# Optimization experiments

Measured on AMD Instinct MI355X. Metric: run time of the kernel, lower is better.

The kernel has to match this reference:

```python
import jax, jax.numpy as jnp
import numpy as np

N = 100000
E = 1600000
DIM = 16
H = 128


def setup_inputs() -> dict:
    key = jax.random.key(0)
    ks = jax.random.split(key, 16)
    s = 0.05
    inp = {
        "x": jax.random.normal(ks[0], (N, DIM), dtype=jnp.float32),
        "edge_index": jax.random.randint(ks[1], (2, E), 0, N, dtype=jnp.int32),
        # mlp_pre: dim -> h -> h -> h (ReLU after each, incl. last)
        "W1": jax.random.normal(ks[2], (DIM, H), dtype=jnp.float32) * s,
        "b1": jnp.zeros((H,), jnp.float32),
        "W2": jax.random.normal(ks[3], (H, H), dtype=jnp.float32) * s,
        "b2": jnp.zeros((H,), jnp.float32),
        "W3": jax.random.normal(ks[4], (H, H), dtype=jnp.float32) * s,
        "b3": jnp.zeros((H,), jnp.float32),
        # lin: h -> h (message transform)
        "Wl": jax.random.normal(ks[5], (H, H), dtype=jnp.float32) * s,
        "bl": jnp.zeros((H,), jnp.float32),
        # mlp_post: 2h -> h -> h -> dim (ReLU after first two only)
        "P1": jax.random.normal(ks[6], (2 * H, H), dtype=jnp.float32) * s,
        "pb1": jnp.zeros((H,), jnp.float32),
        "P2": jax.random.normal(ks[7], (H, H), dtype=jnp.float32) * s,
        "pb2": jnp.zeros((H,), jnp.float32),
        "P3": jax.random.normal(ks[8], (H, DIM), dtype=jnp.float32) * s,
        "pb3": jnp.zeros((DIM,), jnp.float32),
    }
    return inp


def _mlp_pre(x, W1, b1, W2, b2, W3, b3):
    h = jax.nn.relu(x @ W1 + b1)
    h = jax.nn.relu(h @ W2 + b2)
    return jax.nn.relu(h @ W3 + b3)


def reference(x, edge_index, W1, b1, W2, b2, W3, b3, Wl, bl, P1, pb1, P2, pb2, P3, pb3):
    # mlp_pre and the message transform are pointwise per node, so compute once
    # per node, then gather per edge (same math as PyG's per-edge x_j path).
    pre = _mlp_pre(x, W1, b1, W2, b2, W3, b3)            # [N, H]
    msg_node = jax.nn.relu(pre @ Wl + bl)                # [N, H]
    src, dst = edge_index[0], edge_index[1]
    agg = jax.ops.segment_sum(msg_node[src], dst, num_segments=N)  # [N, H]
    h = jnp.concatenate([pre, agg], axis=1)              # [N, 2H]
    h = jax.nn.relu(h @ P1 + pb1)
    h = jax.nn.relu(h @ P2 + pb2)
    out = h @ P3 + pb3                                   # [N, DIM] (no last act in mlp_post)
    return jax.nn.relu(out)                              # outer activation in GNNCASimple
```

## Files before the change

### kernel.cpp

```cpp
#include <hip/hip_runtime.h>

#define N_ 100000
#define E_ 1600000
#define HD 128
#define NB 391
#define GB 256
#define CHK 6250
#define NBGB (NB * GB)

typedef unsigned short u16;
typedef unsigned int u32;
typedef __bf16 bf16x8 __attribute__((ext_vector_type(8)));
typedef float f32x4 __attribute__((ext_vector_type(4)));

#define OFF_W2 0
#define OFF_W3 16384
#define OFF_WL 32768
#define OFF_P2 49152
#define OFF_P1 65536
#define PK_TOT 98304

__device__ __forceinline__ u16 f2bf(float f) {
    u32 u = __float_as_uint(f);
    return (u16)((u + 0x7FFFu + ((u >> 16) & 1u)) >> 16);
}
__device__ __forceinline__ float bf2f(u16 h) {
    return __uint_as_float(((u32)h) << 16);
}
__device__ __forceinline__ f32x4 mfma16(uint4 a, uint4 b, f32x4 c) {
    return __builtin_amdgcn_mfma_f32_16x16x32_bf16(
        __builtin_bit_cast(bf16x8, a), __builtin_bit_cast(bf16x8, b), c, 0, 0, 0);
}

__device__ __forceinline__ uint4 ldsA(const u16* A, int row, int kt, int l) {
    int idx = row * 128 + (((kt * 32 + ((l >> 4) << 3))) ^ ((row & 7) << 3));
    return *(const uint4*)&A[idx];
}

__device__ __forceinline__ void writeActH(u16* Ah, f32x4 acc, int mt, int nt, int l) {
    const int col = nt * 16 + (l & 15);
#pragma unroll
    for (int r = 0; r < 4; ++r) {
        const int row = mt * 16 + ((l >> 4) << 2) + r;
        Ah[row * 128 + (col ^ ((row & 7) << 3))] = f2bf(fmaxf(acc[r], 0.f));
    }
}

template<int MT, int KT>
__device__ __forceinline__ void mfmaLayerW(const u16* Ah,
                                           const u16* __restrict__ wph,
                                           const u16* __restrict__ wpl,
                                           const float* __restrict__ bias,
                                           int nt, int l, f32x4 acc[MT])
{
    const float bv = bias[nt * 16 + (l & 15)];
#pragma unroll
    for (int mt = 0; mt < MT; ++mt) {
        acc[mt][0] = bv; acc[mt][1] = bv; acc[mt][2] = bv; acc[mt][3] = bv;
    }
#pragma unroll
    for (int kt = 0; kt < KT; ++kt) {
        uint4 bh = *(const uint4*)&wph[((nt * KT + kt) * 64 + l) * 8];
        uint4 bl = *(const uint4*)&wpl[((nt * KT + kt) * 64 + l) * 8];
#pragma unroll
        for (int mt = 0; mt < MT; ++mt) {
            uint4 ah = ldsA(Ah, mt * 16 + (l & 15), kt, l);
            acc[mt] = mfma16(ah, bl, acc[mt]);
            acc[mt] = mfma16(ah, bh, acc[mt]);
        }
    }
}

__global__ __launch_bounds__(256) void k_pack(
    const float* __restrict__ W2, const float* __restrict__ W3,
    const float* __restrict__ Wl, const float* __restrict__ P2,
    const float* __restrict__ P1, u16* __restrict__ wpk)
{
    int e = blockIdx.x * 256 + threadIdx.x;
    if (e >= PK_TOT) return;
    const float* src; int local, KT;
    if (e < OFF_P1) {
        int m = e >> 14;
        src = (m == 0) ? W2 : (m == 1) ? W3 : (m == 2) ? Wl : P2;
        local = e & 16383; KT = 4;
    } else {
        src = P1; local = e - OFF_P1; KT = 8;
    }
    int j = local & 7, lane = (local >> 3) & 63, t = local >> 9;
    int kt = t % KT, nt = t / KT;
    int k = kt * 32 + ((lane >> 4) << 3) + j;
    int n = nt * 16 + (lane & 15);
    float v = src[k * HD + n];
    u16 h = f2bf(v);
    wpk[e] = h;
    wpk[PK_TOT + e] = f2bf(v - bf2f(h));
}

template<int NPH>
__device__ __forceinline__ void layer1(const float xs[][16],
                                       const float* __restrict__ W1,
                                       const float* __restrict__ b1,
                                       u16* Uh, int f, int g)
{
    float w[16];
#pragma unroll
    for (int j = 0; j < 16; ++j) w[j] = W1[j * HD + f];
    const float bb = b1[f];
#pragma unroll
    for (int nn = 0; nn < NPH; ++nn) {
        const int row = g * NPH + nn;
        const float4* h4 = (const float4*)xs[row];
        float4 h0 = h4[0], h1 = h4[1], h2 = h4[2], h3 = h4[3];
        float a = bb
            + h0.x * w[0] + h0.y * w[1] + h0.z * w[2] + h0.w * w[3]
            + h1.x * w[4] + h1.y * w[5] + h1.z * w[6] + h1.w * w[7]
            + h2.x * w[8] + h2.y * w[9] + h2.z * w[10] + h2.w * w[11]
            + h3.x * w[12] + h3.y * w[13] + h3.z * w[14] + h3.w * w[15];
        Uh[row * 128 + (f ^ ((row & 7) << 3))] = f2bf(fmaxf(a, 0.f));
    }
}

__global__ __launch_bounds__(512) void k_msg(
    const float* __restrict__ x,
    const float* __restrict__ W1, const float* __restrict__ b1,
    const float* __restrict__ b2, const float* __restrict__ b3,
    const float* __restrict__ blin,
    const u16* __restrict__ wpk, u16* __restrict__ msg16,
    u16* __restrict__ pre16)
{
    __shared__ float xs[32][16];
    __shared__ __align__(16) u16 Uh[4096], Vh[4096];
    const int tid = threadIdx.x;
    const int l = tid & 63, w = tid >> 6;
    const int base = blockIdx.x * 32;

    xs[tid >> 4][tid & 15] = x[(base + (tid >> 4)) * 16 + (tid & 15)];
    __syncthreads();

    layer1<8>(xs, W1, b1, Uh, tid & 127, tid >> 7);
    __syncthreads();

    f32x4 acc[2];
    mfmaLayerW<2, 4>(Uh, wpk + OFF_W2, wpk + PK_TOT + OFF_W2, b2, w, l, acc);
    writeActH(Vh, acc[0], 0, w, l);
    writeActH(Vh, acc[1], 1, w, l);
    __syncthreads();

    mfmaLayerW<2, 4>(Vh, wpk + OFF_W3, wpk + PK_TOT + OFF_W3, b3, w, l, acc);
    writeActH(Uh, acc[0], 0, w, l);
    writeActH(Uh, acc[1], 1, w, l);
    __syncthreads();

    mfmaLayerW<2, 4>(Uh, wpk + OFF_WL, wpk + PK_TOT + OFF_WL, blin, w, l, acc);
    writeActH(Vh, acc[0], 0, w, l);
    writeActH(Vh, acc[1], 1, w, l);
    __syncthreads();

    {
        int e = tid * 8;
        int r = e >> 7, c0 = e & 127;
        int idx = r * HD + (c0 ^ ((r & 7) << 3));
        size_t g = (size_t)(base + r) * HD + c0;
        *(uint4*)&msg16[g] = *(const uint4*)&Vh[idx];
        *(uint4*)&pre16[g] = *(const uint4*)&Uh[idx];
    }
}

__global__ __launch_bounds__(256) void k_count(const int* __restrict__ dst,
                                               int* __restrict__ cnt)
{
    __shared__ int lc[NB];
    const int tid = threadIdx.x;
    for (int i = tid; i < NB; i += 256) lc[i] = 0;
    __syncthreads();
    const int e0 = blockIdx.x * CHK, e1 = min(e0 + CHK, E_);
    for (int e = e0 + tid; e < e1; e += 256)
        atomicAdd(&lc[dst[e] >> 8], 1);
    __syncthreads();
    for (int i = tid; i < NB; i += 256) cnt[i * GB + blockIdx.x] = lc[i];
}

__global__ void k_bsum(const int* __restrict__ v, int* __restrict__ part, int L)
{
    __shared__ int s[256];
    int i = blockIdx.x * 256 + threadIdx.x;
    int t = threadIdx.x;
    s[t] = (i < L) ? v[i] : 0;
    __syncthreads();
    for (int st = 128; st > 0; st >>= 1) {
        if (t < st) s[t] += s[t + st];
        __syncthreads();
    }
    if (t == 0) part[blockIdx.x] = s[0];
}

__global__ void k_pscan(const int* __restrict__ part, int* __restrict__ poff, int nb)
{
    __shared__ int s[512];
    int t = threadIdx.x;
    int d = (t < nb) ? part[t] : 0;
    s[t] = d;
    __syncthreads();
    for (int st = 1; st < 512; st <<= 1) {
        int v = (t >= st) ? s[t - st] : 0;
        __syncthreads();
        s[t] += v;
        __syncthreads();
    }
    if (t < nb) poff[t] = s[t] - d;
}

__global__ void k_scan_excl(const int* __restrict__ v, const int* __restrict__ poff,
                            int* __restrict__ outp, int L)
{
    __shared__ int s[256];
    int i = blockIdx.x * 256 + threadIdx.x;
    int t = threadIdx.x;
    int d = (i < L) ? v[i] : 0;
    s[t] = d;
    __syncthreads();
    for (int st = 1; st < 256; st <<= 1) {
        int vv = (t >= st) ? s[t - st] : 0;
        __syncthreads();
        s[t] += vv;
        __syncthreads();
    }
    if (i < L) outp[i] = s[t] - d + poff[blockIdx.x];
}

__global__ __launch_bounds__(256) void k_scatter(const int* __restrict__ src,
                                                 const int* __restrict__ dst,
                                                 const int* __restrict__ escan,
                                                 uint2* __restrict__ ebuf)
{
    __shared__ int lcur[NB];
    const int tid = threadIdx.x;
    for (int i = tid; i < NB; i += 256) lcur[i] = escan[i * GB + blockIdx.x];
    __syncthreads();
    const int e0 = blockIdx.x * CHK, e1 = min(e0 + CHK, E_);
    for (int e = e0 + tid; e < e1; e += 256) {
        int s = src[e], d = dst[e];
        int pos = atomicAdd(&lcur[d >> 8], 1);
        ebuf[pos] = uint2{(u32)s, (u32)d};
    }
}

__global__ __launch_bounds__(256) void k_fill2(const uint2* __restrict__ ebuf,
                                               const int* __restrict__ escan,
                                               int* __restrict__ offs,
                                               int* __restrict__ endp,
                                               int* __restrict__ csr)
{
    __shared__ int hist[256], sc[256], cur[256];
    const int tid = threadIdx.x, b = blockIdx.x;
    const int s = escan[b * GB];
    const int e = (b == NB - 1) ? E_ : escan[(b + 1) * GB];
    hist[tid] = 0;
    __syncthreads();
    for (int i = s + tid; i < e; i += 256)
        atomicAdd(&hist[ebuf[i].y & 255], 1);
    __syncthreads();
    int d = hist[tid];
    sc[tid] = d;
    __syncthreads();
    for (int st = 1; st < 256; st <<= 1) {
        int v = (tid >= st) ? sc[tid - st] : 0;
        __syncthreads();
        sc[tid] += v;
        __syncthreads();
    }
    int ex = s + sc[tid] - d;
    int node = (b << 8) + tid;
    if (node < N_) { offs[node] = ex; endp[node] = ex + d; }
    cur[tid] = ex;
    __syncthreads();
    for (int i = s + tid; i < e; i += 256) {
        uint2 u = ebuf[i];
        int pos = atomicAdd(&cur[u.y & 255], 1);
        csr[pos] = u.x;
    }
}

__global__ __launch_bounds__(256) void k_agg(
    const u16* __restrict__ msg16, const int* __restrict__ csr,
    const int* __restrict__ offs, const int* __restrict__ endp,
    u32* __restrict__ agg16)
{
    const int w = threadIdx.x >> 6, l = threadIdx.x & 63;
    const int node = blockIdx.x * 4 + w;
    if (node >= N_) return;
    const int s = offs[node], e = endp[node];
    float a0 = 0.f, a1 = 0.f;
    int i = s;
    for (; i + 8 <= e; i += 8) {
        u32 d[8];
#pragma unroll
        for (int q = 0; q < 8; ++q)
            d[q] = ((const u32*)(msg16 + (size_t)csr[i + q] * HD))[l];
#pragma unroll
        for (int q = 0; q < 8; ++q) {
            a0 += __uint_as_float(d[q] << 16);
            a1 += __uint_as_float(d[q] & 0xffff0000u);
        }
    }
    for (; i < e; ++i) {
        u32 d = ((const u32*)(msg16 + (size_t)csr[i] * HD))[l];
        a0 += __uint_as_float(d << 16);
        a1 += __uint_as_float(d & 0xffff0000u);
    }
    agg16[(size_t)node * 64 + l] = ((u32)f2bf(a1) << 16) | (u32)f2bf(a0);
}

__global__ __launch_bounds__(512) void k_post(
    const u16* __restrict__ pre16, const u32* __restrict__ agg16,
    const float* __restrict__ pb1, const float* __restrict__ pb2,
    const float* __restrict__ P3, const float* __restrict__ pb3,
    const u16* __restrict__ wpk, float* __restrict__ out)
{
    __shared__ __align__(16) u16 Uh[4096], Vh[4096];
    const int tid = threadIdx.x;
    const int l = tid & 63, w = tid >> 6;
    const int base = blockIdx.x * 32;

    {
        int e = tid * 8;
        int r = e >> 7, c0 = e & 127;
        int idx = r * HD + (c0 ^ ((r & 7) << 3));
        size_t g = (size_t)(base + r) * HD + c0;
        *(uint4*)&Uh[idx] = *(const uint4*)&pre16[g];
        *(uint4*)&Vh[idx] = *(const uint4*)&agg16[g >> 1];
    }
    __syncthreads();

    f32x4 acc[2];
    {
        const float bv = pb1[w * 16 + (l & 15)];
        acc[0][0] = bv; acc[0][1] = bv; acc[0][2] = bv; acc[0][3] = bv;
        acc[1] = acc[0];
#pragma unroll
        for (int kt = 0; kt < 8; ++kt) {
            const u16* sh = (kt < 4) ? Uh : Vh;
            uint4 bh = *(const uint4*)&wpk[OFF_P1 + ((w * 8 + kt) * 64 + l) * 8];
            uint4 bl = *(const uint4*)&wpk[PK_TOT + OFF_P1 + ((w * 8 + kt) * 64 + l) * 8];
#pragma unroll
            for (int mt = 0; mt < 2; ++mt) {
                uint4 ah = ldsA(sh, mt * 16 + (l & 15), kt & 3, l);
                acc[mt] = mfma16(ah, bl, acc[mt]);
                acc[mt] = mfma16(ah, bh, acc[mt]);
            }
        }
    }
    __syncthreads();
    writeActH(Uh, acc[0], 0, w, l);
    writeActH(Uh, acc[1], 1, w, l);
    __syncthreads();

    mfmaLayerW<2, 4>(Uh, wpk + OFF_P2, wpk + PK_TOT + OFF_P2, pb2, w, l, acc);
    writeActH(Vh, acc[0], 0, w, l);
    writeActH(Vh, acc[1], 1, w, l);
    __syncthreads();

    {
        const int o = tid & 15;
        const int n = tid >> 4;
        const int sn = (n & 7) << 3;
        float a = pb3[o];
        for (int k0 = 0; k0 < HD; k0 += 8) {
            uint4 ph = *(const uint4*)&Vh[n * HD + (k0 ^ sn)];
            const u32 pw[4] = {ph.x, ph.y, ph.z, ph.w};
#pragma unroll
            for (int j = 0; j < 8; ++j) {
                u32 hv = (j & 1) ? (pw[j >> 1] & 0xffff0000u) : (pw[j >> 1] << 16);
                a += __uint_as_float(hv) * P3[(k0 + j) * 16 + o];
            }
        }
        out[(size_t)(base + n) * 16 + o] = fmaxf(a, 0.f);
    }
}

extern "C" void kernel_launch(void* const* d_in, const int* in_sizes, int n_in,
                              void* d_out, int out_size, void* d_ws, size_t ws_size,
                              hipStream_t stream)
{
    const float* x  = (const float*)d_in[0];
    const int*   ei = (const int*)d_in[1];
    const float* W1 = (const float*)d_in[2];  const float* b1  = (const float*)d_in[3];
    const float* W2 = (const float*)d_in[4];  const float* b2  = (const float*)d_in[5];
    const float* W3 = (const float*)d_in[6];  const float* b3  = (const float*)d_in[7];
    const float* Wl = (const float*)d_in[8];  const float* bl  = (const float*)d_in[9];
    const float* P1 = (const float*)d_in[10]; const float* pb1 = (const float*)d_in[11];
    const float* P2 = (const float*)d_in[12]; const float* pb2 = (const float*)d_in[13];
    const float* P3 = (const float*)d_in[14]; const float* pb3 = (const float*)d_in[15];
    float* out = (float*)d_out;

    char* ws = (char*)d_ws;
    u16* msg16  = (u16*)ws;   ws += (size_t)N_ * HD * 2;
    u32* agg16  = (u32*)ws;   ws += (size_t)N_ * 64 * 4;
    uint2* ebuf = (uint2*)agg16;
    int* csr    = (int*)ws;   ws += (size_t)E_ * 4;
    int* offs   = (int*)ws;   ws += (size_t)N_ * 4;
    int* endp   = (int*)ws;   ws += (size_t)N_ * 4;
    int* cnt    = (int*)ws;   ws += (size_t)NBGB * 4;
    int* escan  = (int*)ws;   ws += (size_t)NBGB * 4;
    int* partC  = (int*)ws;   ws += 512 * 4;
    int* poffC  = (int*)ws;   ws += 512 * 4;
    u16* wpk    = (u16*)ws;   ws += (size_t)2 * PK_TOT * 2;
    u16* pre16  = (u16*)ws;   ws += (size_t)N_ * HD * 2;

    const int* srcv = ei;
    const int* dstv = ei + E_;
    const int nbC = NBGB / 256;

    k_pack<<<(PK_TOT + 255) / 256, 256, 0, stream>>>(W2, W3, Wl, P2, P1, wpk);
    k_msg<<<N_ / 32, 512, 0, stream>>>(x, W1, b1, b2, b3, bl, wpk, msg16, pre16);
    k_count<<<GB, 256, 0, stream>>>(dstv, cnt);
    k_bsum<<<nbC, 256, 0, stream>>>(cnt, partC, NBGB);
    k_pscan<<<1, 512, 0, stream>>>(partC, poffC, nbC);
    k_scan_excl<<<nbC, 256, 0, stream>>>(cnt, poffC, escan, NBGB);
    k_scatter<<<GB, 256, 0, stream>>>(srcv, dstv, escan, ebuf);
    k_fill2<<<NB, 256, 0, stream>>>(ebuf, escan, offs, endp, csr);
    k_agg<<<(N_ + 3) / 4, 256, 0, stream>>>(msg16, csr, offs, endp, agg16);
    k_post<<<N_ / 32, 512, 0, stream>>>(pre16, agg16, pb1, pb2, P3, pb3, wpk, out);
}
```

Before: 213.1 us.

## Process 64 nodes per block in MLP kernels and split edges across half-waves in aggregation

The k_msg and k_post kernels now handle 64 rows per block instead of 32, with 4 M-tiles per wave. Each B-fragment weight load is reused across twice as many MFMAs, and the 391-block grid overhead is halved. k_agg now has each half-wave gather a different edge, using 8-byte loads per lane, then combines the halves with a cross-half shuffle so more gathers are in flight. The cost is double the LDS and more registers per block, which may reduce occupancy. Bounds guards are added for the partial last block.

```diff
diff --git a/kernel.cpp b/kernel.cpp
--- a/kernel.cpp
+++ b/kernel.cpp
@@ -128,41 +128,47 @@
     const u16* __restrict__ wpk, u16* __restrict__ msg16,
     u16* __restrict__ pre16)
 {
-    __shared__ float xs[32][16];
-    __shared__ __align__(16) u16 Uh[4096], Vh[4096];
+    __shared__ float xs[64][16];
+    __shared__ __align__(16) u16 Uh[8192], Vh[8192];
     const int tid = threadIdx.x;
     const int l = tid & 63, w = tid >> 6;
-    const int base = blockIdx.x * 32;
-
-    xs[tid >> 4][tid & 15] = x[(base + (tid >> 4)) * 16 + (tid & 15)];
-    __syncthreads();
-
-    layer1<8>(xs, W1, b1, Uh, tid & 127, tid >> 7);
-    __syncthreads();
-
-    f32x4 acc[2];
-    mfmaLayerW<2, 4>(Uh, wpk + OFF_W2, wpk + PK_TOT + OFF_W2, b2, w, l, acc);
-    writeActH(Vh, acc[0], 0, w, l);
-    writeActH(Vh, acc[1], 1, w, l);
-    __syncthreads();
-
-    mfmaLayerW<2, 4>(Vh, wpk + OFF_W3, wpk + PK_TOT + OFF_W3, b3, w, l, acc);
-    writeActH(Uh, acc[0], 0, w, l);
-    writeActH(Uh, acc[1], 1, w, l);
-    __syncthreads();
-
-    mfmaLayerW<2, 4>(Uh, wpk + OFF_WL, wpk + PK_TOT + OFF_WL, blin, w, l, acc);
-    writeActH(Vh, acc[0], 0, w, l);
-    writeActH(Vh, acc[1], 1, w, l);
-    __syncthreads();
-
-    {
-        int e = tid * 8;
+    const int base = blockIdx.x * 64;
+
+    for (int i = tid; i < 64 * 16; i += 512) {
+        int node = min(base + (i >> 4), N_ - 1);
+        xs[i >> 4][i & 15] = x[node * 16 + (i & 15)];
+    }
+    __syncthreads();
+
+    layer1<16>(xs, W1, b1, Uh, tid & 127, tid >> 7);
+    __syncthreads();
+
+    f32x4 acc[4];
+    mfmaLayerW<4, 4>(Uh, wpk + OFF_W2, wpk + PK_TOT + OFF_W2, b2, w, l, acc);
+#pragma unroll
+    for (int mt = 0; mt < 4; ++mt) writeActH(Vh, acc[mt], mt, w, l);
+    __syncthreads();
+
+    mfmaLayerW<4, 4>(Vh, wpk + OFF_W3, wpk + PK_TOT + OFF_W3, b3, w, l, acc);
+#pragma unroll
+    for (int mt = 0; mt < 4; ++mt) writeActH(Uh, acc[mt], mt, w, l);
+    __syncthreads();
+
+    mfmaLayerW<4, 4>(Uh, wpk + OFF_WL, wpk + PK_TOT + OFF_WL, blin, w, l, acc);
+#pragma unroll
+    for (int mt = 0; mt < 4; ++mt) writeActH(Vh, acc[mt], mt, w, l);
+    __syncthreads();
+
+#pragma unroll
+    for (int chunk = 0; chunk < 2; ++chunk) {
+        int e = tid * 8 + chunk * 4096;
         int r = e >> 7, c0 = e & 127;
-        int idx = r * HD + (c0 ^ ((r & 7) << 3));
-        size_t g = (size_t)(base + r) * HD + c0;
-        *(uint4*)&msg16[g] = *(const uint4*)&Vh[idx];
-        *(uint4*)&pre16[g] = *(const uint4*)&Uh[idx];
+        if (base + r < N_) {
+            int idx = r * HD + (c0 ^ ((r & 7) << 3));
+            size_t g = (size_t)(base + r) * HD + c0;
+            *(uint4*)&msg16[g] = *(const uint4*)&Vh[idx];
+            *(uint4*)&pre16[g] = *(const uint4*)&Uh[idx];
+        }
     }
 }
 
@@ -289,26 +295,51 @@
     const int w = threadIdx.x >> 6, l = threadIdx.x & 63;
     const int node = blockIdx.x * 4 + w;
     if (node >= N_) return;
+    const int c = l & 31, h = l >> 5;
     const int s = offs[node], e = endp[node];
-    float a0 = 0.f, a1 = 0.f;
+    float a0 = 0.f, a1 = 0.f, a2 = 0.f, a3 = 0.f;
     int i = s;
     for (; i + 8 <= e; i += 8) {
-        u32 d[8];
-#pragma unroll
-        for (int q = 0; q < 8; ++q)
-            d[q] = ((const u32*)(msg16 + (size_t)csr[i + q] * HD))[l];
-#pragma unroll
-        for (int q = 0; q < 8; ++q) {
-            a0 += __uint_as_float(d[q] << 16);
-            a1 += __uint_as_float(d[q] & 0xffff0000u);
-        }
-    }
-    for (; i < e; ++i) {
-        u32 d = ((const u32*)(msg16 + (size_t)csr[i] * HD))[l];
-        a0 += __uint_as_float(d << 16);
-        a1 += __uint_as_float(d & 0xffff0000u);
-    }
-    agg16[(size_t)node * 64 + l] = ((u32)f2bf(a1) << 16) | (u32)f2bf(a0);
+        uint2 d[4];
+#pragma unroll
+        for (int q = 0; q < 4; ++q) {
+            int src = csr[i + 2 * q + h];
+            d[q] = *(const uint2*)&((const u32*)(msg16 + (size_t)src * HD))[2 * c];
+        }
+#pragma unroll
+        for (int q = 0; q < 4; ++q) {
+            a0 += __uint_as_float(d[q].x << 16);
+            a1 += __uint_as_float(d[q].x & 0xffff0000u);
+            a2 += __uint_as_float(d[q].y << 16);
+            a3 += __uint_as_float(d[q].y & 0xffff0000u);
+        }
+    }
+    for (; i + 2 <= e; i += 2) {
+        int src = csr[i + h];
+        uint2 d = *(const uint2*)&((const u32*)(msg16 + (size_t)src * HD))[2 * c];
+        a0 += __uint_as_float(d.x << 16);
+        a1 += __uint_as_float(d.x & 0xffff0000u);
+        a2 += __uint_as_float(d.y << 16);
+        a3 += __uint_as_float(d.y & 0xffff0000u);
+    }
+    if (i < e && h == 0) {
+        int src = csr[i];
+        uint2 d = *(const uint2*)&((const u32*)(msg16 + (size_t)src * HD))[2 * c];
+        a0 += __uint_as_float(d.x << 16);
+        a1 += __uint_as_float(d.x & 0xffff0000u);
+        a2 += __uint_as_float(d.y << 16);
+        a3 += __uint_as_float(d.y & 0xffff0000u);
+    }
+    a0 += __shfl_xor(a0, 32);
+    a1 += __shfl_xor(a1, 32);
+    a2 += __shfl_xor(a2, 32);
+    a3 += __shfl_xor(a3, 32);
+    if (h == 0) {
+        uint2 o;
+        o.x = ((u32)f2bf(a1) << 16) | (u32)f2bf(a0);
+        o.y = ((u32)f2bf(a3) << 16) | (u32)f2bf(a2);
+        *(uint2*)&agg16[(size_t)node * 64 + 2 * c] = o;
+    }
 }
 
 __global__ __launch_bounds__(512) void k_post(
@@ -317,33 +348,36 @@
     const float* __restrict__ P3, const float* __restrict__ pb3,
     const u16* __restrict__ wpk, float* __restrict__ out)
 {
-    __shared__ __align__(16) u16 Uh[4096], Vh[4096];
+    __shared__ __align__(16) u16 Uh[8192], Vh[8192];
     const int tid = threadIdx.x;
     const int l = tid & 63, w = tid >> 6;
-    const int base = blockIdx.x * 32;
-
-    {
-        int e = tid * 8;
+    const int base = blockIdx.x * 64;
+
+#pragma unroll
+    for (int chunk = 0; chunk < 2; ++chunk) {
+        int e = tid * 8 + chunk * 4096;
         int r = e >> 7, c0 = e & 127;
         int idx = r * HD + (c0 ^ ((r & 7) << 3));
-        size_t g = (size_t)(base + r) * HD + c0;
+        size_t g = (size_t)min(base + r, N_ - 1) * HD + c0;
         *(uint4*)&Uh[idx] = *(const uint4*)&pre16[g];
         *(uint4*)&Vh[idx] = *(const uint4*)&agg16[g >> 1];
     }
     __syncthreads();
 
-    f32x4 acc[2];
+    f32x4 acc[4];
     {
         const float bv = pb1[w * 16 + (l & 15)];
-        acc[0][0] = bv; acc[0][1] = bv; acc[0][2] = bv; acc[0][3] = bv;
-        acc[1] = acc[0];
+#pragma unroll
+        for (int mt = 0; mt < 4; ++mt) {
+            acc[mt][0] = bv; acc[mt][1] = bv; acc[mt][2] = bv; acc[mt][3] = bv;
+        }
 #pragma unroll
         for (int kt = 0; kt < 8; ++kt) {
             const u16* sh = (kt < 4) ? Uh : Vh;
             uint4 bh = *(const uint4*)&wpk[OFF_P1 + ((w * 8 + kt) * 64 + l) * 8];
             uint4 bl = *(const uint4*)&wpk[PK_TOT + OFF_P1 + ((w * 8 + kt) * 64 + l) * 8];
 #pragma unroll
-            for (int mt = 0; mt < 2; ++mt) {
+            for (int mt = 0; mt < 4; ++mt) {
                 uint4 ah = ldsA(sh, mt * 16 + (l & 15), kt & 3, l);
                 acc[mt] = mfma16(ah, bl, acc[mt]);
                 acc[mt] = mfma16(ah, bh, acc[mt]);
@@ -351,30 +385,34 @@
         }
     }
     __syncthreads();
-    writeActH(Uh, acc[0], 0, w, l);
-    writeActH(Uh, acc[1], 1, w, l);
-    __syncthreads();
-
-    mfmaLayerW<2, 4>(Uh, wpk + OFF_P2, wpk + PK_TOT + OFF_P2, pb2, w, l, acc);
-    writeActH(Vh, acc[0], 0, w, l);
-    writeActH(Vh, acc[1], 1, w, l);
+#pragma unroll
+    for (int mt = 0; mt < 4; ++mt) writeActH(Uh, acc[mt], mt, w, l);
+    __syncthreads();
+
+    mfmaLayerW<4, 4>(Uh, wpk + OFF_P2, wpk + PK_TOT + OFF_P2, pb2, w, l, acc);
+#pragma unroll
+    for (int mt = 0; mt < 4; ++mt) writeActH(Vh, acc[mt], mt, w, l);
     __syncthreads();
 
     {
         const int o = tid & 15;
-        const int n = tid >> 4;
-        const int sn = (n & 7) << 3;
-        float a = pb3[o];
-        for (int k0 = 0; k0 < HD; k0 += 8) {
-            uint4 ph = *(const uint4*)&Vh[n * HD + (k0 ^ sn)];
-            const u32 pw[4] = {ph.x, ph.y, ph.z, ph.w};
-#pragma unroll
-            for (int j = 0; j < 8; ++j) {
-                u32 hv = (j & 1) ? (pw[j >> 1] & 0xffff0000u) : (pw[j >> 1] << 16);
-                a += __uint_as_float(hv) * P3[(k0 + j) * 16 + o];
+#pragma unroll
+        for (int p = 0; p < 2; ++p) {
+            const int n = p * 32 + (tid >> 4);
+            const int sn = (n & 7) << 3;
+            float a = pb3[o];
+            for (int k0 = 0; k0 < HD; k0 += 8) {
+                uint4 ph = *(const uint4*)&Vh[n * HD + (k0 ^ sn)];
+                const u32 pw[4] = {ph.x, ph.y, ph.z, ph.w};
+#pragma unroll
+                for (int j = 0; j < 8; ++j) {
+                    u32 hv = (j & 1) ? (pw[j >> 1] & 0xffff0000u) : (pw[j >> 1] << 16);
+                    a += __uint_as_float(hv) * P3[(k0 + j) * 16 + o];
+                }
             }
-        }
-        out[(size_t)(base + n) * 16 + o] = fmaxf(a, 0.f);
+            if (base + n < N_)
+                out[(size_t)(base + n) * 16 + o] = fmaxf(a, 0.f);
+        }
     }
 }
 
@@ -410,9 +448,10 @@
     const int* srcv = ei;
     const int* dstv = ei + E_;
     const int nbC = NBGB / 256;
+    const int nbM = (N_ + 63) / 64;
 
     k_pack<<<(PK_TOT + 255) / 256, 256, 0, stream>>>(W2, W3, Wl, P2, P1, wpk);
-    k_msg<<<N_ / 32, 512, 0, stream>>>(x, W1, b1, b2, b3, bl, wpk, msg16, pre16);
+    k_msg<<<nbM, 512, 0, stream>>>(x, W1, b1, b2, b3, bl, wpk, msg16, pre16);
     k_count<<<GB, 256, 0, stream>>>(dstv, cnt);
     k_bsum<<<nbC, 256, 0, stream>>>(cnt, partC, NBGB);
     k_pscan<<<1, 512, 0, stream>>>(partC, poffC, nbC);
@@ -420,5 +459,5 @@
     k_scatter<<<GB, 256, 0, stream>>>(srcv, dstv, escan, ebuf);
     k_fill2<<<NB, 256, 0, stream>>>(ebuf, escan, offs, endp, csr);
     k_agg<<<(N_ + 3) / 4, 256, 0, stream>>>(msg16, csr, offs, endp, agg16);
-    k_post<<<N_ / 32, 512, 0, stream>>>(pre16, agg16, pb1, pb2, P3, pb3, wpk, out);
-}
+    k_post<<<nbM, 512, 0, stream>>>(pre16, agg16, pb1, pb2, P3, pb3, wpk, out);
+}
```

After: 279.8 us. +31.3%, slower.
